# Kernel optimization log

Hardware: AMD Instinct MI355X
Metric: run time of the kernel (lower is better)

Reference implementation:

```python
import jax, jax.numpy as jnp
import numpy as np

LN_EPS = 1e-5
NEG_INF = -1e38


def wkv_scan(w, u, k, v):
    """Numerically-stable RWKV WKV recurrence (matches wkv_cuda forward).
    w: [C] (negative decay), u: [C] bonus, k/v: [B,T,C]. Returns y: [B,T,C]."""
    Bdim, T, C = k.shape

    def step(carry, kv_t):
        p, q, o = carry  # running num, den, log-scale, each [B,C]
        kt, vt = kv_t
        no = jnp.maximum(o, u + kt)
        A = jnp.exp(o - no)
        Bw = jnp.exp(u + kt - no)
        y = (A * p + Bw * vt) / (A * q + Bw)
        no2 = jnp.maximum(w + o, kt)
        A2 = jnp.exp(w + o - no2)
        B2 = jnp.exp(kt - no2)
        return (A2 * p + B2 * vt, A2 * q + B2, no2), y

    init = (jnp.zeros((Bdim, C), k.dtype), jnp.zeros((Bdim, C), k.dtype),
            jnp.full((Bdim, C), NEG_INF, k.dtype))
    kT = jnp.moveaxis(k, 1, 0)  # [T,B,C]
    vT = jnp.moveaxis(v, 1, 0)
    _, ys = jax.lax.scan(step, init, (kT, vT))
    return jnp.moveaxis(ys, 0, 1)  # [B,T,C]


def setup_inputs() -> dict:
    key = jax.random.key(0)
    ks = jax.random.split(key, 8)
    B, C, H, W = 16, 192, 56, 56
    s = 0.02
    x = jax.random.normal(ks[0], (B, C, H, W), jnp.float32)
    Wk = jax.random.normal(ks[1], (C, C), jnp.float32) * s
    Wv = jax.random.normal(ks[2], (C, C), jnp.float32) * s
    Wr = jax.random.normal(ks[3], (C, C), jnp.float32) * s
    Wo = jax.random.normal(ks[4], (C, C), jnp.float32) * s
    ln_g = jnp.ones((C,), jnp.float32)
    ln_b = jnp.zeros((C,), jnp.float32)
    w_decay = -6.0 + 0.1 * jax.random.normal(ks[5], (C,), jnp.float32)
    u = 0.1 * jax.random.normal(ks[6], (C,), jnp.float32)
    return {"x": x, "Wk": Wk, "Wv": Wv, "Wr": Wr, "Wo": Wo,
            "ln_g": ln_g, "ln_b": ln_b, "w_decay": w_decay, "u": u}


def reference(x, Wk, Wv, Wr, Wo, ln_g, ln_b, w_decay, u):
    B, C, H, W = x.shape
    xs = jnp.transpose(x.reshape(B, C, H * W), (0, 2, 1))  # [B,T,C]
    k = jnp.einsum('btc,dc->btd', xs, Wk)
    v = jnp.einsum('btc,dc->btd', xs, Wv)
    r = jnp.einsum('btc,dc->btd', xs, Wr)
    real_w = -jnp.exp(w_decay)
    x_fwd = wkv_scan(real_w, u, k, v)
    x_bwd = jnp.flip(wkv_scan(real_w, u, jnp.flip(k, 1), jnp.flip(v, 1)), 1)
    x_bi = 0.5 * (x_fwd + x_bwd)
    h = jax.nn.sigmoid(r) * x_bi
    mu = jnp.mean(h, axis=-1, keepdims=True)
    var = jnp.var(h, axis=-1, keepdims=True)
    h = (h - mu) * jax.lax.rsqrt(var + LN_EPS) * ln_g + ln_b
    out = jnp.einsum('btc,dc->btd', h, Wo)  # dropout is identity at eval
    return jnp.transpose(out, (0, 2, 1)).reshape(B, C, H, W)
```

## Files before the change

kernel.cpp:

```cpp
#include <hip/hip_runtime.h>
#include <hip/hip_bf16.h>

#define BB 16
#define CC 192
#define TPIX 3136
#define NCH 49
#define CHL 64
#define NNELE ((size_t)BB * TPIX * CC)
#define NSTATE ((size_t)2 * BB * NCH * CC)
#define WCH (CC * CC)
#define NROWS ((size_t)BB * TPIX)

typedef __attribute__((ext_vector_type(8))) short bf16x8;
typedef __attribute__((ext_vector_type(4))) float f32x4;
typedef __attribute__((ext_vector_type(16))) float f32x16;

__device__ __forceinline__ unsigned short f2bf(float f) {
    __hip_bfloat16 b = __float2bfloat16(f);
    return *reinterpret_cast<unsigned short*>(&b);
}
__device__ __forceinline__ float bf2f(unsigned short h) {
    union { unsigned u; float f; } v; v.u = ((unsigned)h) << 16;
    return v.f;
}


__global__ __launch_bounds__(256) void wcvt_frag(
    const float* __restrict__ Wk, const float* __restrict__ Wv,
    const float* __restrict__ Wr, const float* __restrict__ Wo,
    const float* __restrict__ gamma,
    unsigned short* __restrict__ wfrag)
{
    const int id = blockIdx.x * 256 + threadIdx.x;
    const int m = id / 4608;
    const int r = id % 4608;
    const int tile = r >> 6;
    const int lane = r & 63;
    const int dr = tile / 12, tk = tile % 12;
    const int d = dr * 32 + (lane & 31);
    const int c = tk * 16 + (lane >> 5) * 8;
    const float* W = (m == 0) ? Wk : (m == 1) ? Wv : (m == 2) ? Wr : Wo;
    const float4 a = *(const float4*)&W[d * CC + c];
    const float4 b = *(const float4*)&W[d * CC + c + 4];
    float g[8];
#pragma unroll
    for (int i = 0; i < 8; ++i) g[i] = (m == 3) ? gamma[c + i] : 1.f;
    bf16x8 o;
    o[0] = (short)f2bf(a.x * g[0]); o[1] = (short)f2bf(a.y * g[1]);
    o[2] = (short)f2bf(a.z * g[2]); o[3] = (short)f2bf(a.w * g[3]);
    o[4] = (short)f2bf(b.x * g[4]); o[5] = (short)f2bf(b.y * g[5]);
    o[6] = (short)f2bf(b.z * g[6]); o[7] = (short)f2bf(b.w * g[7]);
    *(bf16x8*)&wfrag[(size_t)m * WCH + (size_t)tile * 512 + lane * 8] = o;
}

__global__ __launch_bounds__(192) void wgb_kernel(
    const float* __restrict__ Wo, const float* __restrict__ gamma,
    const float* __restrict__ beta,
    float* __restrict__ Wg, float* __restrict__ Wb)
{
    const int d = threadIdx.x;
    float sg = 0.f, sb = 0.f;
    for (int c = 0; c < CC; c += 4) {
        const float4 w = *(const float4*)&Wo[d * CC + c];
        const float4 g = *(const float4*)&gamma[c];
        const float4 bb = *(const float4*)&beta[c];
        sg += w.x * g.x + w.y * g.y + w.z * g.z + w.w * g.w;
        sb += w.x * bb.x + w.y * bb.y + w.z * bb.z + w.w * bb.w;
    }
    Wg[d] = sg; Wb[d] = sb;
}

__global__ __launch_bounds__(256) void xcvt_frag(
    const float* __restrict__ x, unsigned short* __restrict__ xfrag)
{
    const int t0 = blockIdx.x * 32;
    const int b  = blockIdx.y;
    __shared__ float ls[CC][33];
    const int tid = threadIdx.x;
#pragma unroll
    for (int it = 0; it < 6; ++it) {
        const int c  = it * 32 + (tid >> 3);
        const int t4 = (tid & 7) * 4;
        *(float4*)&ls[c][t4] =
            *(const float4*)&x[((size_t)b * CC + c) * TPIX + t0 + t4];
    }
    __syncthreads();
    const size_t tbase = ((size_t)(b * TPIX + t0) >> 5) * 12;
#pragma unroll
    for (int it = 0; it < 3; ++it) {
        const int id = it * 256 + tid;
        const int tk = id >> 6;
        const int lane = id & 63;
        const int r32 = lane & 31;
        const int c0 = tk * 16 + (lane >> 5) * 8;
        bf16x8 o;
#pragma unroll
        for (int e = 0; e < 8; ++e)
            o[e] = (short)f2bf(ls[c0 + e][r32]);
        *(bf16x8*)&xfrag[(tbase + tk) * 512 + lane * 8] = o;
    }
}

__global__ __launch_bounds__(512, 4) void proj_mfma32(
    const unsigned short* __restrict__ xfrag,
    const unsigned short* __restrict__ wfrag,
    unsigned short* __restrict__ kbf, unsigned short* __restrict__ vbf,
    unsigned short* __restrict__ rfrag)
{
    __shared__ unsigned short wlds[WCH];
    const int tid  = threadIdx.x;
    const int lane = tid & 63;
    const int wv   = tid >> 6;
    const int tw   = wv >> 1;
    const int dwav = wv & 1;
    const int l31  = lane & 31;
    const int kh   = lane >> 5;
    const int m    = blockIdx.z;

    const size_t row0 = (size_t)blockIdx.x * 128 + tw * 32;
    const size_t xtb  = (row0 >> 5) * 12;

    bf16x8 xf[12];
#pragma unroll
    for (int ks = 0; ks < 12; ++ks)
        xf[ks] = *(const bf16x8*)&xfrag[(xtb + ks) * 512 + lane * 8];

    const unsigned short* wm = wfrag + (size_t)m * WCH;
#pragma unroll
    for (int it = 0; it < 9; ++it) {
        const int off = (it * 512 + tid) * 8;
        *(bf16x8*)&wlds[off] = *(const bf16x8*)&wm[off];
    }
    __syncthreads();

    f32x16 acc[3];
#pragma unroll
    for (int nn = 0; nn < 3; ++nn)
#pragma unroll
        for (int e = 0; e < 16; ++e) acc[nn][e] = 0.f;

#pragma unroll
    for (int ks = 0; ks < 12; ++ks) {
        bf16x8 wf[3];
#pragma unroll
        for (int nn = 0; nn < 3; ++nn)
            wf[nn] = *(const bf16x8*)&wlds[((dwav * 3 + nn) * 12 + ks) * 512 + lane * 8];
#pragma unroll
        for (int nn = 0; nn < 3; ++nn)
            acc[nn] = __builtin_amdgcn_mfma_f32_32x32x16_bf16(
                xf[ks], wf[nn], acc[nn], 0, 0, 0);
    }

    if (m == 2) {
#pragma unroll
        for (int nn = 0; nn < 3; ++nn) {
            const int d = dwav * 96 + nn * 32 + l31;
            const size_t tb = ((row0 >> 5) * 12 + (d >> 4)) * 512 +
                              (size_t)(((d >> 3) & 1) * 32) * 8 + (d & 7);
#pragma unroll
            for (int q = 0; q < 16; ++q) {
                const int tq = (q & 3) + 8 * (q >> 2) + 4 * kh;
                rfrag[tb + tq * 8] = f2bf(acc[nn][q]);
            }
        }
    } else {
        unsigned short* om = (m == 0) ? kbf : vbf;
#pragma unroll
        for (int nn = 0; nn < 3; ++nn) {
            const int d = dwav * 96 + nn * 32 + l31;
#pragma unroll
            for (int q = 0; q < 16; ++q) {
                const int t = (q & 3) + 8 * (q >> 2) + 4 * kh;
                om[(row0 + t) * CC + d] = f2bf(acc[nn][q]);
            }
        }
    }
}

__global__ __launch_bounds__(256) void wkv_chunk_kernel(
    const unsigned short* __restrict__ kb, const unsigned short* __restrict__ vb,
    const float* __restrict__ wdec,
    float* __restrict__ sp, float* __restrict__ sq, float* __restrict__ so)
{
    const int gid = blockIdx.x * 256 + threadIdx.x;
    const int c  = gid % CC;
    const int r  = gid / CC;
    const int ch = r % NCH;
    const int r2 = r / NCH;
    const int b  = r2 % BB;
    const int dir = r2 / BB;

    const float w = -__expf(wdec[c]);
    const int tstart = dir ? (TPIX - 1 - ch * CHL) : (ch * CHL);
    const long stride = dir ? -(long)CC : (long)CC;
    long idx = ((long)b * TPIX + tstart) * CC + c;

    float p = 0.f, q = 0.f, o = -1e38f;
#pragma unroll 4
    for (int j = 0; j < CHL; ++j) {
        const float kt = bf2f(kb[idx]), vt = bf2f(vb[idx]);
        const float wo  = w + o;
        const float no2 = fmaxf(wo, kt);
        const float A2  = __expf(wo - no2);
        const float B2  = __expf(kt - no2);
        p = A2 * p + B2 * vt;
        q = A2 * q + B2;
        o = no2;
        idx += stride;
    }
    sp[gid] = p; sq[gid] = q; so[gid] = o;
}

__global__ __launch_bounds__(256) void wkv_prefix_kernel(
    float* __restrict__ sp, float* __restrict__ sq, float* __restrict__ so,
    const float* __restrict__ wdec)
{
    const int tid = blockIdx.x * 256 + threadIdx.x;
    if (tid >= 2 * BB * CC) return;
    const int c = tid % CC;
    const int g = tid / CC;
    const float w  = -__expf(wdec[c]);
    const float wL = w * CHL;

    float P = 0.f, Q = 0.f, O = -1e38f;
    size_t idx = (size_t)g * NCH * CC + c;
    for (int ch = 0; ch < NCH; ++ch) {
        const float pl = sp[idx], ql = sq[idx], ol = so[idx];
        sp[idx] = P; sq[idx] = Q; so[idx] = O;
        const float Ow = O + wL;
        const float no = fmaxf(Ow, ol);
        const float A  = __expf(Ow - no);
        const float Bf = __expf(ol - no);
        P = A * P + Bf * pl;
        Q = A * Q + Bf * ql;
        O = no;
        idx += CC;
    }
}

__global__ __launch_bounds__(256) void wkv_emit_kernel(
    const unsigned short* __restrict__ kb, const unsigned short* __restrict__ vb,
    const float* __restrict__ wdec, const float* __restrict__ ubias,
    const float* __restrict__ sp, const float* __restrict__ sq,
    const float* __restrict__ so,
    unsigned short* __restrict__ yfwd, unsigned short* __restrict__ ybwd)
{
    const int gid = blockIdx.x * 256 + threadIdx.x;
    const int c  = gid % CC;
    const int r  = gid / CC;
    const int ch = r % NCH;
    const int r2 = r / NCH;
    const int b  = r2 % BB;
    const int dir = r2 / BB;

    const float w = -__expf(wdec[c]);
    const float u = ubias[c];
    const int tstart = dir ? (TPIX - 1 - ch * CHL) : (ch * CHL);
    const long stride = dir ? -(long)CC : (long)CC;
    const int rstep = dir ? -1 : 1;
    long idx = ((long)b * TPIX + tstart) * CC + c;
    long row = (long)b * TPIX + tstart;
    unsigned short* yout = dir ? ybwd : yfwd;
    const int ctile = c >> 4;
    const int clane = ((c >> 3) & 1) * 32;
    const int ce    = c & 7;

    float p = sp[gid], q = sq[gid], o = so[gid];
#pragma unroll 2
    for (int j = 0; j < CHL; ++j) {
        const float kt = bf2f(kb[idx]), vt = bf2f(vb[idx]);
        const float uk  = u + kt;
        const float no  = fmaxf(o, uk);
        const float A   = __expf(o - no);
        const float Bw  = __expf(uk - no);
        const float num = A * p + Bw * vt;
        const float den = A * q + Bw;
        const size_t off = ((size_t)(row >> 5) * 12 + ctile) * 512 +
                           (size_t)((row & 31) + clane) * 8 + ce;
        yout[off] = f2bf(0.5f * __fdividef(num, den));
        const float wo  = w + o;
        const float no2 = fmaxf(wo, kt);
        const float A2  = __expf(wo - no2);
        const float B2  = __expf(kt - no2);
        p = A2 * p + B2 * vt;
        q = A2 * q + B2;
        o = no2;
        idx += stride;
        row += rstep;
    }
}

__global__ __launch_bounds__(512) void outproj_ln_mfma32(
    const unsigned short* __restrict__ yfwd, const unsigned short* __restrict__ ybwd,
    const unsigned short* __restrict__ rfrag,
    const float* __restrict__ Wg, const float* __restrict__ Wb,
    const unsigned short* __restrict__ wo,
    float* __restrict__ out)
{
    __shared__ unsigned short wlds[WCH];
    const int tid  = threadIdx.x;
    const int lane = tid & 63;
    const int wv   = tid >> 6;
    const int tw   = wv >> 1;
    const int dwav = wv & 1;
    const int l31  = lane & 31;
    const int kh   = lane >> 5;

    const size_t row0 = (size_t)blockIdx.x * 128 + tw * 32;
    const size_t htb  = (row0 >> 5) * 12;

#pragma unroll
    for (int it = 0; it < 9; ++it) {
        const int off = (it * 512 + tid) * 8;
        *(bf16x8*)&wlds[off] = *(const bf16x8*)&wo[off];
    }
    __syncthreads();

    bf16x8 ones;
#pragma unroll
    for (int e = 0; e < 8; ++e) ones[e] = (short)0x3F80;

    f32x16 acc[3], accs, accs2;
#pragma unroll
    for (int nn = 0; nn < 3; ++nn)
#pragma unroll
        for (int e = 0; e < 16; ++e) acc[nn][e] = 0.f;
#pragma unroll
    for (int e = 0; e < 16; ++e) { accs[e] = 0.f; accs2[e] = 0.f; }

#pragma unroll
    for (int ks = 0; ks < 12; ++ks) {
        const size_t fo = (htb + ks) * 512 + lane * 8;
        const bf16x8 yf = *(const bf16x8*)&yfwd[fo];
        const bf16x8 yb = *(const bf16x8*)&ybwd[fo];
        const bf16x8 rv = *(const bf16x8*)&rfrag[fo];
        bf16x8 hb, hq;
#pragma unroll
        for (int e = 0; e < 8; ++e) {
            const float xb = bf2f((unsigned short)yf[e]) + bf2f((unsigned short)yb[e]);
            const float rr = bf2f((unsigned short)rv[e]);
            const float h  = __fdividef(xb, 1.f + __expf(-rr));
            hb[e] = (short)f2bf(h);
            hq[e] = (short)f2bf(h * h);
        }
        bf16x8 wf[3];
#pragma unroll
        for (int nn = 0; nn < 3; ++nn)
            wf[nn] = *(const bf16x8*)&wlds[((dwav * 3 + nn) * 12 + ks) * 512 + lane * 8];
#pragma unroll
        for (int nn = 0; nn < 3; ++nn)
            acc[nn] = __builtin_amdgcn_mfma_f32_32x32x16_bf16(
                hb, wf[nn], acc[nn], 0, 0, 0);
        accs  = __builtin_amdgcn_mfma_f32_32x32x16_bf16(hb, ones, accs, 0, 0, 0);
        accs2 = __builtin_amdgcn_mfma_f32_32x32x16_bf16(hq, ones, accs2, 0, 0, 0);
    }

    float muv[16], rsv[16];
#pragma unroll
    for (int q = 0; q < 16; ++q) {
        const float mu  = accs[q] * (1.f / CC);
        const float var = accs2[q] * (1.f / CC) - mu * mu;
        muv[q] = mu;
        rsv[q] = rsqrtf(var + 1e-5f);
    }

#pragma unroll
    for (int nn = 0; nn < 3; ++nn) {
        const int d = dwav * 96 + nn * 32 + l31;
        const float wg = Wg[d];
        const float wb = Wb[d];
#pragma unroll
        for (int q2 = 0; q2 < 4; ++q2) {
            const size_t grow = row0 + 4 * kh + 8 * q2;
            const int b  = (int)(grow / TPIX);
            const int tl = (int)(grow % TPIX);
            f32x4 v4;
#pragma unroll
            for (int j = 0; j < 4; ++j) {
                const int q = q2 * 4 + j;
                v4[j] = rsv[q] * (acc[nn][q] - muv[q] * wg) + wb;
            }
            *(f32x4*)&out[((size_t)b * CC + d) * TPIX + tl] = v4;
        }
    }
}

extern "C" void kernel_launch(void* const* d_in, const int* in_sizes, int n_in,
                              void* d_out, int out_size, void* d_ws, size_t ws_size,
                              hipStream_t stream)
{
    const float* x    = (const float*)d_in[0];
    const float* Wk   = (const float*)d_in[1];
    const float* Wv   = (const float*)d_in[2];
    const float* Wr   = (const float*)d_in[3];
    const float* Wo   = (const float*)d_in[4];
    const float* ln_g = (const float*)d_in[5];
    const float* ln_b = (const float*)d_in[6];
    const float* wdec = (const float*)d_in[7];
    const float* u    = (const float*)d_in[8];

    unsigned short* kbf   = (unsigned short*)d_ws;
    unsigned short* vbf   = kbf + NNELE;
    unsigned short* rfrag = vbf + NNELE;
    unsigned short* xfrag = rfrag + NNELE;
    unsigned short* wfrag = xfrag + NNELE;
    unsigned short* yfwd  = wfrag + 4 * WCH;
    unsigned short* ybwd  = yfwd + NNELE;
    float* Wg_buf = (float*)(ybwd + NNELE);
    float* Wb_buf = Wg_buf + CC;
    float* sp = (float*)xfrag;
    float* sq = sp + NSTATE;
    float* so = sq + NSTATE;
    float* out = (float*)d_out;

    wcvt_frag<<<72, 256, 0, stream>>>(Wk, Wv, Wr, Wo, ln_g, wfrag);
    wgb_kernel<<<1, 192, 0, stream>>>(Wo, ln_g, ln_b, Wg_buf, Wb_buf);
    xcvt_frag<<<dim3(TPIX / 32, BB), 256, 0, stream>>>(x, xfrag);

    proj_mfma32<<<dim3((BB * TPIX) / 128, 1, 3), 512, 0, stream>>>(
        xfrag, wfrag, kbf, vbf, rfrag);

    const int nth = (int)NSTATE;
    wkv_chunk_kernel<<<nth / 256, 256, 0, stream>>>(kbf, vbf, wdec, sp, sq, so);
    wkv_prefix_kernel<<<(2 * BB * CC + 255) / 256, 256, 0, stream>>>(sp, sq, so, wdec);
    wkv_emit_kernel<<<nth / 256, 256, 0, stream>>>(kbf, vbf, wdec, u, sp, sq, so, yfwd, ybwd);

    outproj_ln_mfma32<<<(BB * TPIX) / 128, 512, 0, stream>>>(
        yfwd, ybwd, rfrag, Wg_buf, Wb_buf, wfrag + 3 * WCH, out);
}
```

Before: 136.0 us.

## Prefetch activations into registers and compute LN stats with shuffles instead of MFMA

Loads all twelve y_fwd/y_bwd/r fragments into registers before staging the weight tile to LDS, so the global loads overlap the LDS fill and barrier. LayerNorm row sums and sums of squares are now accumulated per lane in fp32 and reduced with cross-half shuffles, then redistributed with shuffles. This replaces the two extra MFMAs against a ones vector and their accumulators, and it keeps the stats in full precision rather than rounding h*h to bf16. Launch bounds request two blocks per CU, which raises register pressure against the 36 prefetched fragment registers and may cause spills.

```diff
diff --git a/kernel.cpp b/kernel.cpp
--- a/kernel.cpp
+++ b/kernel.cpp
@@ -290,7 +290,7 @@
     }
 }
 
-__global__ __launch_bounds__(512) void outproj_ln_mfma32(
+__global__ __launch_bounds__(512, 2) void outproj_ln_mfma32(
     const unsigned short* __restrict__ yfwd, const unsigned short* __restrict__ ybwd,
     const unsigned short* __restrict__ rfrag,
     const float* __restrict__ Wg, const float* __restrict__ Wb,
@@ -309,6 +309,15 @@
     const size_t row0 = (size_t)blockIdx.x * 128 + tw * 32;
     const size_t htb  = (row0 >> 5) * 12;
 
+    bf16x8 yf[12], yb[12], rv[12];
+#pragma unroll
+    for (int ks = 0; ks < 12; ++ks) {
+        const size_t fo = (htb + ks) * 512 + lane * 8;
+        yf[ks] = *(const bf16x8*)&yfwd[fo];
+        yb[ks] = *(const bf16x8*)&ybwd[fo];
+        rv[ks] = *(const bf16x8*)&rfrag[fo];
+    }
+
 #pragma unroll
     for (int it = 0; it < 9; ++it) {
         const int off = (it * 512 + tid) * 8;
@@ -316,32 +325,24 @@
     }
     __syncthreads();
 
-    bf16x8 ones;
-#pragma unroll
-    for (int e = 0; e < 8; ++e) ones[e] = (short)0x3F80;
-
-    f32x16 acc[3], accs, accs2;
+    f32x16 acc[3];
 #pragma unroll
     for (int nn = 0; nn < 3; ++nn)
 #pragma unroll
         for (int e = 0; e < 16; ++e) acc[nn][e] = 0.f;
-#pragma unroll
-    for (int e = 0; e < 16; ++e) { accs[e] = 0.f; accs2[e] = 0.f; }
-
+
+    float s = 0.f, s2 = 0.f;
 #pragma unroll
     for (int ks = 0; ks < 12; ++ks) {
-        const size_t fo = (htb + ks) * 512 + lane * 8;
-        const bf16x8 yf = *(const bf16x8*)&yfwd[fo];
-        const bf16x8 yb = *(const bf16x8*)&ybwd[fo];
-        const bf16x8 rv = *(const bf16x8*)&rfrag[fo];
-        bf16x8 hb, hq;
+        bf16x8 hb;
 #pragma unroll
         for (int e = 0; e < 8; ++e) {
-            const float xb = bf2f((unsigned short)yf[e]) + bf2f((unsigned short)yb[e]);
-            const float rr = bf2f((unsigned short)rv[e]);
+            const float xb = bf2f((unsigned short)yf[ks][e]) +
+                             bf2f((unsigned short)yb[ks][e]);
+            const float rr = bf2f((unsigned short)rv[ks][e]);
             const float h  = __fdividef(xb, 1.f + __expf(-rr));
+            s += h; s2 += h * h;
             hb[e] = (short)f2bf(h);
-            hq[e] = (short)f2bf(h * h);
         }
         bf16x8 wf[3];
 #pragma unroll
@@ -351,17 +352,20 @@
         for (int nn = 0; nn < 3; ++nn)
             acc[nn] = __builtin_amdgcn_mfma_f32_32x32x16_bf16(
                 hb, wf[nn], acc[nn], 0, 0, 0);
-        accs  = __builtin_amdgcn_mfma_f32_32x32x16_bf16(hb, ones, accs, 0, 0, 0);
-        accs2 = __builtin_amdgcn_mfma_f32_32x32x16_bf16(hq, ones, accs2, 0, 0, 0);
-    }
+    }
+
+    s  += __shfl_xor(s, 32);
+    s2 += __shfl_xor(s2, 32);
+    const float mu   = s * (1.f / CC);
+    const float var  = s2 * (1.f / CC) - mu * mu;
+    const float rstd = rsqrtf(var + 1e-5f);
 
     float muv[16], rsv[16];
 #pragma unroll
     for (int q = 0; q < 16; ++q) {
-        const float mu  = accs[q] * (1.f / CC);
-        const float var = accs2[q] * (1.f / CC) - mu * mu;
-        muv[q] = mu;
-        rsv[q] = rsqrtf(var + 1e-5f);
+        const int tq = (q & 3) + 8 * (q >> 2) + 4 * kh;
+        muv[q] = __shfl(mu, tq);
+        rsv[q] = __shfl(rstd, tq);
     }
 
 #pragma unroll
```

Measured after the change: 137.8 us. About the same (+1.3%).
